# Performance work log

Hardware: AMD Instinct MI355X
Metric: run time of the kernel (lower is better)

## Reference

```python
import jax, jax.numpy as jnp
import numpy as np


def setup_inputs() -> dict:
    key = jax.random.key(0)
    T, B, N = 2048, 16, 2048
    spikes = (jax.random.uniform(key, (T, B, N)) < 0.05).astype(jnp.float32)
    return {"input_spikes": spikes, "duration": 100}


def reference(input_spikes, duration):
    # Causal sliding-window (boxcar) sum over the time axis of length `duration`,
    # equivalent to conv1d with a ones kernel and causal padding, then clamp to [0,1].
    # psp[t] = clip( sum_{k=max(0,t-duration+1)}^{t} x[k], 0, 1 )
    T = input_spikes.shape[0]
    c = jnp.cumsum(input_spikes, axis=0)                     # [T, ...]
    pad = [(duration, 0)] + [(0, 0)] * (input_spikes.ndim - 1)
    c_shift = jnp.pad(c, pad)[:T]                            # c[t-duration], 0 for t<duration
    win = c - c_shift
    return jnp.clip(win, 0.0, 1.0)
```

## Files before the change

### kernel.cpp

```cpp
#include <hip/hip_runtime.h>


#define T_TOTAL 2048
#define M_COLS  (16 * 2048)
#define CHUNK   256

__global__ __launch_bounds__(256) void psp_scan_kernel(
    const float* __restrict__ x,
    const int*  __restrict__ dur_p,
    float* __restrict__ out)
{
    const int col = blockIdx.x * blockDim.x + threadIdx.x;
    const int t0  = blockIdx.y * CHUNK;
    const int duration = dur_p[0];

    int last = t0 - duration;

    int tstart = t0 - duration + 1;
    if (tstart < 0) tstart = 0;

    const float* xc = x + col;
    float* oc = out + col;

    for (int t = tstart; t < t0; ++t) {
        float v = xc[t * M_COLS];
        if (v != 0.0f) last = t;
    }

    #pragma unroll 4
    for (int t = t0; t < t0 + CHUNK; ++t) {
        float v = xc[t * M_COLS];
        if (v != 0.0f) last = t;
        oc[t * M_COLS] = (t - last < duration) ? 1.0f : 0.0f;
    }
}

extern "C" void kernel_launch(void* const* d_in, const int* in_sizes, int n_in,
                              void* d_out, int out_size, void* d_ws, size_t ws_size,
                              hipStream_t stream) {
    const float* x     = (const float*)d_in[0];
    const int*   dur_p = (const int*)d_in[1];
    float*       out   = (float*)d_out;

    dim3 grid(M_COLS / 256, T_TOTAL / CHUNK);
    dim3 block(256);
    psp_scan_kernel<<<grid, block, 0, stream>>>(x, dur_p, out);
}
```

Baseline: 451.4 us.

## Pack spikes into bitmaps and compute window via log-step OR scan

Replaces the per-column serial scan with three kernels. The first packs the float spike train into a 1-bit-per-element bitmap using vector loads and wave shuffles. The second computes the causal window OR over bitmap words in LDS with a doubling scan, using a 104-row halo. The third expands the bitmap back to floats with nontemporal vector stores. The aim is to cut the halo re-reads and the per-thread serial dependency, at the cost of two extra launches and a workspace requirement. The LDS halo path only covers durations up to about 168; larger values would index out of range.

```diff
diff --git a/kernel.cpp b/kernel.cpp
--- a/kernel.cpp
+++ b/kernel.cpp
@@ -2,35 +2,129 @@
 
 
 #define T_TOTAL 2048
-#define M_COLS  (16 * 2048)
-#define CHUNK   256
+#define B_DIM   16
+#define N_DIM   2048
+#define M_COLS  (B_DIM * N_DIM)
+#define MW      (M_COLS / 32)
+#define BM_WORDS ((long long)T_TOTAL * MW)
+#define BM_BYTES (BM_WORDS * 4)
 
-__global__ __launch_bounds__(256) void psp_scan_kernel(
-    const float* __restrict__ x,
-    const int*  __restrict__ dur_p,
+typedef float v4f __attribute__((ext_vector_type(4)));
+
+__global__ __launch_bounds__(256) void binarize_kernel(
+    const float* __restrict__ x, unsigned* __restrict__ bm)
+{
+    const long long total8 = (long long)T_TOTAL * M_COLS / 8;
+    const int gid = blockIdx.x * blockDim.x + threadIdx.x;
+    const int gsz = gridDim.x * blockDim.x;
+    for (long long g = gid; g < total8; g += gsz) {
+        const v4f* p = (const v4f*)(x + g * 8);
+        v4f a = p[0], b = p[1];
+        unsigned byte =
+            (a.x != 0.f ?   1u : 0u) | (a.y != 0.f ?   2u : 0u) |
+            (a.z != 0.f ?   4u : 0u) | (a.w != 0.f ?   8u : 0u) |
+            (b.x != 0.f ?  16u : 0u) | (b.y != 0.f ?  32u : 0u) |
+            (b.z != 0.f ?  64u : 0u) | (b.w != 0.f ? 128u : 0u);
+        unsigned my = byte << (8 * (threadIdx.x & 3));
+        my |= __shfl_xor(my, 1);
+        my |= __shfl_xor(my, 2);
+        if ((threadIdx.x & 3) == 0) bm[g >> 2] = my;
+    }
+}
+
+#define TCHUNK 128
+#define HALO   104
+#define ROWS   (TCHUNK + HALO)
+#define WTILE  32
+
+__global__ __launch_bounds__(256) void window_or_kernel(
+    const unsigned* __restrict__ bm, unsigned* __restrict__ obm,
+    const int* __restrict__ dur_p)
+{
+    __shared__ unsigned A[ROWS][WTILE];
+    __shared__ unsigned Bf[ROWS][WTILE];
+    const int w0  = blockIdx.x * WTILE;
+    const int t0  = blockIdx.y * TCHUNK;
+    const int dur = dur_p[0];
+
+    for (int idx = threadIdx.x; idx < ROWS * WTILE; idx += 256) {
+        const int lr = idx / WTILE, w = idx % WTILE;
+        const int tg = t0 - HALO + lr;
+        A[lr][w] = (tg >= 0) ? bm[(long long)tg * MW + w0 + w] : 0u;
+    }
+    __syncthreads();
+
+#define LEVEL(SRC, DST, D)                                            \
+    for (int idx = threadIdx.x; idx < ROWS * WTILE; idx += 256) {     \
+        const int lr = idx / WTILE, w = idx % WTILE;                  \
+        unsigned v = SRC[lr][w];                                      \
+        if (lr >= D) v |= SRC[lr - D][w];                             \
+        DST[lr][w] = v;                                               \
+    }                                                                 \
+    __syncthreads();
+
+    LEVEL(A, Bf, 1)
+    LEVEL(Bf, A, 2)
+    LEVEL(A, Bf, 4)
+    LEVEL(Bf, A, 8)
+    LEVEL(A, Bf, 16)
+    LEVEL(Bf, A, 32)
+#undef LEVEL
+
+    for (int idx = threadIdx.x; idx < TCHUNK * WTILE; idx += 256) {
+        const int r = idx / WTILE, w = idx % WTILE;
+        const int lr = HALO + r;
+        unsigned v;
+        if (dur >= 65) {
+            v = A[lr][w] | A[lr - (dur - 64)][w];
+        } else if (dur >= 33) {
+            v = Bf[lr][w] | Bf[lr - (dur - 32)][w];
+        } else {
+            v = 0u;
+            const int tg = t0 + r;
+            for (int k = 0; k < dur && k <= tg; ++k)
+                v |= bm[(long long)(tg - k) * MW + w0 + w];
+        }
+        obm[(long long)(t0 + r) * MW + w0 + w] = v;
+    }
+}
+
+__global__ __launch_bounds__(256) void expand_kernel(
+    const unsigned* __restrict__ obm, float* __restrict__ out)
+{
+    const long long total4 = (long long)T_TOTAL * M_COLS / 4;
+    const int gid = blockIdx.x * blockDim.x + threadIdx.x;
+    const int gsz = gridDim.x * blockDim.x;
+    for (long long q = gid; q < total4; q += gsz) {
+        const unsigned word = obm[q >> 3];
+        const unsigned b = (word >> ((q & 7) * 4)) & 0xFu;
+        v4f o;
+        o.x = (b & 1u) ? 1.f : 0.f;
+        o.y = (b & 2u) ? 1.f : 0.f;
+        o.z = (b & 4u) ? 1.f : 0.f;
+        o.w = (b & 8u) ? 1.f : 0.f;
+        __builtin_nontemporal_store(o, (v4f*)out + q);
+    }
+}
+
+#define FCHUNK 256
+__global__ __launch_bounds__(256) void psp_scan_fallback(
+    const float* __restrict__ x, const int* __restrict__ dur_p,
     float* __restrict__ out)
 {
     const int col = blockIdx.x * blockDim.x + threadIdx.x;
-    const int t0  = blockIdx.y * CHUNK;
+    const int t0  = blockIdx.y * FCHUNK;
     const int duration = dur_p[0];
-
     int last = t0 - duration;
-
     int tstart = t0 - duration + 1;
     if (tstart < 0) tstart = 0;
-
     const float* xc = x + col;
     float* oc = out + col;
-
-    for (int t = tstart; t < t0; ++t) {
-        float v = xc[t * M_COLS];
-        if (v != 0.0f) last = t;
-    }
-
+    for (int t = tstart; t < t0; ++t)
+        if (xc[t * M_COLS] != 0.0f) last = t;
     #pragma unroll 4
-    for (int t = t0; t < t0 + CHUNK; ++t) {
-        float v = xc[t * M_COLS];
-        if (v != 0.0f) last = t;
+    for (int t = t0; t < t0 + FCHUNK; ++t) {
+        if (xc[t * M_COLS] != 0.0f) last = t;
         oc[t * M_COLS] = (t - last < duration) ? 1.0f : 0.0f;
     }
 }
@@ -42,7 +136,14 @@
     const int*   dur_p = (const int*)d_in[1];
     float*       out   = (float*)d_out;
 
-    dim3 grid(M_COLS / 256, T_TOTAL / CHUNK);
-    dim3 block(256);
-    psp_scan_kernel<<<grid, block, 0, stream>>>(x, dur_p, out);
+    if (d_ws != nullptr && ws_size >= (size_t)(2 * BM_BYTES)) {
+        unsigned* bm  = (unsigned*)d_ws;
+        unsigned* obm = bm + BM_WORDS;
+        binarize_kernel<<<dim3(2048), dim3(256), 0, stream>>>(x, bm);
+        window_or_kernel<<<dim3(MW / WTILE, T_TOTAL / TCHUNK), dim3(256), 0, stream>>>(bm, obm, dur_p);
+        expand_kernel<<<dim3(2048), dim3(256), 0, stream>>>(obm, out);
+    } else {
+        dim3 grid(M_COLS / 256, T_TOTAL / FCHUNK);
+        psp_scan_fallback<<<grid, dim3(256), 0, stream>>>(x, dur_p, out);
+    }
 }
```

Result: slower. 468.9 us (+3.9%).

## Replace per-column time scan with cooperative bitmask pack, windowed OR, expand

Applied to the files above, without the earlier changes.

Adds a cooperative kernel in three phases separated by grid-wide syncs. First it packs the binary spikes into a per-timestep bitmask with wave ballots, storing it in the output buffer as scratch. Then each block ORs the bitmask rows in its duration window into shared memory. Finally it expands those bits to floats with vectorised nontemporal stores. This is meant to replace strided scalar loads and the redundant window re-reads with coalesced vector traffic. In exchange it relies on cooperative launch residency, two grid syncs and heavy re-reading of the small bitmask from cache, and falls back to the old scan kernel if the launch fails.

```diff
diff --git a/kernel.cpp b/kernel.cpp
--- a/kernel.cpp
+++ b/kernel.cpp
@@ -1,36 +1,88 @@
 #include <hip/hip_runtime.h>
+#include <hip/hip_cooperative_groups.h>
 
 
 #define T_TOTAL 2048
 #define M_COLS  (16 * 2048)
-#define CHUNK   256
+#define SEG_ROW (M_COLS / 256)
+#define NSEG    ((long long)T_TOTAL * SEG_ROW)
+#define WPR     (M_COLS / 32)
 
-__global__ __launch_bounds__(256) void psp_scan_kernel(
+typedef float v4f __attribute__((ext_vector_type(4)));
+typedef unsigned long long u64;
+typedef unsigned u32;
+
+namespace cg = cooperative_groups;
+
+__global__ __launch_bounds__(256, 8) void psp_coop_kernel(
     const float* __restrict__ x,
     const int*  __restrict__ dur_p,
     float* __restrict__ out)
 {
+    cg::grid_group grid = cg::this_grid();
+    u32* bm = (u32*)out;
+    const int lane  = threadIdx.x & 63;
+    const int wiblk = threadIdx.x >> 6;
+    const long long nwaves = (long long)gridDim.x * 4;
+    const long long wid    = (long long)blockIdx.x * 4 + wiblk;
+
+    for (long long s = wid; s < NSEG; s += nwaves) {
+        v4f v = ((const v4f*)(x + s * 256))[lane];
+        u64 b0 = __ballot(v.x != 0.0f);
+        u64 b1 = __ballot(v.y != 0.0f);
+        u64 b2 = __ballot(v.z != 0.0f);
+        u64 b3 = __ballot(v.w != 0.0f);
+        if (lane < 4) {
+            u64 q = lane == 0 ? b0 : lane == 1 ? b1 : lane == 2 ? b2 : b3;
+            ((u64*)(bm + s * 8))[lane] = q;
+        }
+    }
+    grid.sync();
+
+    __shared__ u32 obm[WPR];
+    const int b   = blockIdx.x;
+    const int dur = dur_p[0];
+    int kmax = dur - 1; if (kmax > b) kmax = b;
+    uint4 acc = make_uint4(0u, 0u, 0u, 0u);
+    for (int k = 0; k <= kmax; ++k) {
+        const uint4 v = ((const uint4*)(bm + (long long)(b - k) * WPR))[threadIdx.x];
+        acc.x |= v.x; acc.y |= v.y; acc.z |= v.z; acc.w |= v.w;
+    }
+    ((uint4*)obm)[threadIdx.x] = acc;
+    grid.sync();
+
+    float* orow = out + (long long)b * M_COLS;
+    for (int g = wiblk; g < SEG_ROW; g += 4) {
+        const u64* qp = (const u64*)(obm + g * 8);
+        u64 q0 = qp[0], q1 = qp[1], q2 = qp[2], q3 = qp[3];
+        v4f o;
+        o.x = ((q0 >> lane) & 1ull) ? 1.0f : 0.0f;
+        o.y = ((q1 >> lane) & 1ull) ? 1.0f : 0.0f;
+        o.z = ((q2 >> lane) & 1ull) ? 1.0f : 0.0f;
+        o.w = ((q3 >> lane) & 1ull) ? 1.0f : 0.0f;
+        __builtin_nontemporal_store(o, (v4f*)(orow + g * 256) + lane);
+    }
+}
+
+#define FCHUNK 256
+__global__ __launch_bounds__(256) void psp_scan_fallback(
+    const float* __restrict__ x, const int* __restrict__ dur_p,
+    float* __restrict__ out)
+{
     const int col = blockIdx.x * blockDim.x + threadIdx.x;
-    const int t0  = blockIdx.y * CHUNK;
+    const int t0  = blockIdx.y * FCHUNK;
     const int duration = dur_p[0];
-
     int last = t0 - duration;
-
     int tstart = t0 - duration + 1;
     if (tstart < 0) tstart = 0;
-
     const float* xc = x + col;
     float* oc = out + col;
-
-    for (int t = tstart; t < t0; ++t) {
-        float v = xc[t * M_COLS];
-        if (v != 0.0f) last = t;
-    }
-
     #pragma unroll 4
-    for (int t = t0; t < t0 + CHUNK; ++t) {
-        float v = xc[t * M_COLS];
-        if (v != 0.0f) last = t;
+    for (int t = tstart; t < t0; ++t)
+        if (xc[t * M_COLS] != 0.0f) last = t;
+    #pragma unroll 4
+    for (int t = t0; t < t0 + FCHUNK; ++t) {
+        if (xc[t * M_COLS] != 0.0f) last = t;
         oc[t * M_COLS] = (t - last < duration) ? 1.0f : 0.0f;
     }
 }
@@ -42,7 +94,12 @@
     const int*   dur_p = (const int*)d_in[1];
     float*       out   = (float*)d_out;
 
-    dim3 grid(M_COLS / 256, T_TOTAL / CHUNK);
-    dim3 block(256);
-    psp_scan_kernel<<<grid, block, 0, stream>>>(x, dur_p, out);
+    void* args[] = {(void*)&x, (void*)&dur_p, (void*)&out};
+    hipError_t e = hipLaunchCooperativeKernel((const void*)psp_coop_kernel,
+                                              dim3(T_TOTAL), dim3(256),
+                                              args, 0, stream);
+    if (e != hipSuccess) {
+        dim3 grid(M_COLS / 256, T_TOTAL / FCHUNK);
+        psp_scan_fallback<<<grid, dim3(256), 0, stream>>>(x, dur_p, out);
+    }
 }
```

Result: slower. 956.4 us (+111.9%).
